# Kernel tuning notes

Measured on AMD Instinct MI355X. Metric: run time of the kernel, lower is better.

## Reference

```python
import jax, jax.numpy as jnp
import numpy as np
import math


def _alibi_slopes(n_heads):
    ratio = 2.0 ** (-8.0 / n_heads)
    return jnp.asarray([ratio ** i for i in range(1, n_heads + 1)], dtype=jnp.float32)


def setup_inputs() -> dict:
    key = jax.random.key(0)
    k1, k2, k3 = jax.random.split(key, 3)
    B, T, D = 2, 2048, 1024
    x = jax.random.normal(k1, (B, T, D), dtype=jnp.float32)
    W_qkv = jax.random.normal(k2, (3 * D, D), dtype=jnp.float32) * (1.0 / math.sqrt(D))
    W_out = jax.random.normal(k3, (D, D), dtype=jnp.float32) * (1.0 / math.sqrt(D))
    return {"x": x, "W_qkv": W_qkv, "W_out": W_out, "n_heads": 16}


def reference(x, W_qkv, W_out, n_heads):
    B, T, D = x.shape
    H = n_heads
    hd = D // H
    scale = 1.0 / math.sqrt(hd)

    # qkv projection: torch Linear computes x @ W.T ; W_qkv is [3D, D]
    qkv = jnp.einsum('btd,ed->bte', x, W_qkv)            # [B, T, 3D]
    qkv = qkv.reshape(B, T, 3, H, hd)
    q = jnp.transpose(qkv[:, :, 0], (0, 2, 1, 3))        # [B, H, T, hd]
    k = jnp.transpose(qkv[:, :, 1], (0, 2, 1, 3))
    v = jnp.transpose(qkv[:, :, 2], (0, 2, 1, 3))

    attn = jnp.einsum('bhqd,bhkd->bhqk', q, k) * scale   # [B, H, T, T]

    pos = jnp.arange(T)
    dist = jnp.abs(pos[None, :] - pos[:, None])          # [T, T]
    slopes = _alibi_slopes(H)                            # [H]
    attn = attn - slopes[None, :, None, None] * dist[None, None, :, :]

    causal = pos[None, :] > pos[:, None]                 # True above diagonal
    attn = jnp.where(causal[None, None, :, :], -jnp.inf, attn)
    attn = jax.nn.softmax(attn, axis=-1)

    out = jnp.einsum('bhqk,bhkd->bhqd', attn, v)         # [B, H, T, hd]
    out = jnp.transpose(out, (0, 2, 1, 3)).reshape(B, T, D)
    return jnp.einsum('btd,ed->bte', out, W_out)         # out projection
```

## Files before the change

### kernel.cpp

```cpp
#include <hip/hip_runtime.h>
#include <hip/hip_bf16.h>
#include <stdint.h>

typedef __attribute__((ext_vector_type(8))) short bf16x8;
typedef __attribute__((ext_vector_type(4))) short short4v;
typedef __attribute__((ext_vector_type(4))) float f32x4;

#define DEV static __device__ __forceinline__

DEV void load_lds16(const void* g, void* l) {
  __builtin_amdgcn_global_load_lds((const __attribute__((address_space(1))) char*)g,
                                   (__attribute__((address_space(3))) char*)l, 16, 0, 0);
}

DEV short f32_to_bf16_bits(float x) {
  union { __hip_bfloat16 h; short s; } u;
  u.h = __float2bfloat16(x);
  return u.s;
}
DEV float bf16_bits_to_f32(short s) {
  union { float f; unsigned u; } u;
  u.u = ((unsigned)(unsigned short)s) << 16;
  return u.f;
}

template<int CTRL>
DEV float dpp_fmax(float x) {
  union { float f; int i; } u, v;
  u.f = x;
  v.i = __builtin_amdgcn_update_dpp(0, u.i, CTRL, 0xf, 0xf, true);
  return fmaxf(x, v.f);
}
DEV float row16_max(float x) {
  x = dpp_fmax<0xB1>(x);
  x = dpp_fmax<0x4E>(x);
  x = dpp_fmax<0x124>(x);
  x = dpp_fmax<0x128>(x);
  return x;
}

#define NX4 1048576
#define NQ4 786432
#define NW4 262144
__global__ __launch_bounds__(256) void conv_f32_bf16(const float4* __restrict__ x,
                                                     const float4* __restrict__ wq,
                                                     const float4* __restrict__ wo,
                                                     short4v* __restrict__ ox,
                                                     short4v* __restrict__ oq,
                                                     short4v* __restrict__ ow) {
  int i = blockIdx.x * 256 + threadIdx.x;
  const float4* src; short4v* dst; int j;
  if (i < NX4)            { src = x;  dst = ox; j = i; }
  else if (i < NX4 + NQ4) { src = wq; dst = oq; j = i - NX4; }
  else                    { src = wo; dst = ow; j = i - NX4 - NQ4; }
  float4 v = src[j];
  short4v s;
  s[0] = f32_to_bf16_bits(v.x); s[1] = f32_to_bf16_bits(v.y);
  s[2] = f32_to_bf16_bits(v.z); s[3] = f32_to_bf16_bits(v.w);
  dst[j] = s;
}

template<bool CF32>
__global__ __launch_bounds__(256) void gemm_bt(const __hip_bfloat16* __restrict__ A,
                                               const __hip_bfloat16* __restrict__ Bt,
                                               void* __restrict__ Cp,
                                               int M, int N, int K) {
  __shared__ short sA[128 * 64];
  __shared__ short sB[128 * 64];
  const int tid = threadIdx.x;
  const int lane = tid & 63;
  const int w = tid >> 6;
  const int wr = w >> 1, wc = w & 1;
  const int l15 = lane & 15, l4 = lane >> 4;
  const long m0 = (long)blockIdx.y * 128, n0 = (long)blockIdx.x * 128;

  f32x4 acc[4][4] = {};

  for (int k0 = 0; k0 < K; k0 += 64) {
    __syncthreads();
#pragma unroll
    for (int c = 0; c < 4; ++c) {
      int ci = c * 256 + tid;
      int row = ci >> 3;
      int sc = (ci & 7) ^ (row & 7);
      load_lds16(A + (m0 + row) * (long)K + k0 + sc * 8, (char*)sA + c * 4096 + w * 1024);
    }
#pragma unroll
    for (int c = 0; c < 4; ++c) {
      int ci = c * 256 + tid;
      int row = ci >> 3;
      int sc = (ci & 7) ^ (row & 7);
      load_lds16(Bt + (n0 + row) * (long)K + k0 + sc * 8, (char*)sB + c * 4096 + w * 1024);
    }
    __syncthreads();
#pragma unroll
    for (int ks = 0; ks < 2; ++ks) {
      bf16x8 av[4], bv[4];
#pragma unroll
      for (int i = 0; i < 4; ++i) {
        int row = wr * 64 + i * 16 + l15;
        int ch = (ks * 4 + l4) ^ (row & 7);
        av[i] = *(const bf16x8*)((const char*)sA + row * 128 + ch * 16);
      }
#pragma unroll
      for (int i = 0; i < 4; ++i) {
        int row = wc * 64 + i * 16 + l15;
        int ch = (ks * 4 + l4) ^ (row & 7);
        bv[i] = *(const bf16x8*)((const char*)sB + row * 128 + ch * 16);
      }
#pragma unroll
      for (int mi = 0; mi < 4; ++mi)
#pragma unroll
        for (int ni = 0; ni < 4; ++ni)
          acc[mi][ni] = __builtin_amdgcn_mfma_f32_16x16x32_bf16(av[mi], bv[ni], acc[mi][ni], 0, 0, 0);
    }
  }
#pragma unroll
  for (int mi = 0; mi < 4; ++mi)
#pragma unroll
    for (int r = 0; r < 4; ++r) {
      long row = m0 + wr * 64 + mi * 16 + l4 * 4 + r;
#pragma unroll
      for (int ni = 0; ni < 4; ++ni) {
        long col = n0 + wc * 64 + ni * 16 + l15;
        if constexpr (CF32)
          ((float*)Cp)[row * (long)N + col] = acc[mi][ni][r];
        else
          ((__hip_bfloat16*)Cp)[row * (long)N + col] = __float2bfloat16(acc[mi][ni][r]);
      }
    }
}

__global__ __launch_bounds__(256) void gemm_bt64(const __hip_bfloat16* __restrict__ A,
                                                 const __hip_bfloat16* __restrict__ Bt,
                                                 float* __restrict__ C,
                                                 int M, int N, int K) {
  __shared__ short sA[64 * 64];
  __shared__ short sB[128 * 64];
  const int tid = threadIdx.x;
  const int lane = tid & 63;
  const int w = tid >> 6;
  const int l15 = lane & 15, l4 = lane >> 4;
  const long m0 = (long)blockIdx.y * 64, n0 = (long)blockIdx.x * 128;

  f32x4 acc[4][2] = {};

  for (int k0 = 0; k0 < K; k0 += 64) {
    __syncthreads();
#pragma unroll
    for (int c = 0; c < 2; ++c) {
      int ci = c * 256 + tid;
      int row = ci >> 3;
      int sc = (ci & 7) ^ (row & 7);
      load_lds16(A + (m0 + row) * (long)K + k0 + sc * 8, (char*)sA + c * 4096 + w * 1024);
    }
#pragma unroll
    for (int c = 0; c < 4; ++c) {
      int ci = c * 256 + tid;
      int row = ci >> 3;
      int sc = (ci & 7) ^ (row & 7);
      load_lds16(Bt + (n0 + row) * (long)K + k0 + sc * 8, (char*)sB + c * 4096 + w * 1024);
    }
    __syncthreads();
#pragma unroll
    for (int ks = 0; ks < 2; ++ks) {
      bf16x8 av[4], bv[2];
#pragma unroll
      for (int i = 0; i < 4; ++i) {
        int row = i * 16 + l15;
        int ch = (ks * 4 + l4) ^ (row & 7);
        av[i] = *(const bf16x8*)((const char*)sA + row * 128 + ch * 16);
      }
#pragma unroll
      for (int i = 0; i < 2; ++i) {
        int row = w * 32 + i * 16 + l15;
        int ch = (ks * 4 + l4) ^ (row & 7);
        bv[i] = *(const bf16x8*)((const char*)sB + row * 128 + ch * 16);
      }
#pragma unroll
      for (int mi = 0; mi < 4; ++mi)
#pragma unroll
        for (int ni = 0; ni < 2; ++ni)
          acc[mi][ni] = __builtin_amdgcn_mfma_f32_16x16x32_bf16(av[mi], bv[ni], acc[mi][ni], 0, 0, 0);
    }
  }
#pragma unroll
  for (int mi = 0; mi < 4; ++mi)
#pragma unroll
    for (int r = 0; r < 4; ++r) {
      long row = m0 + mi * 16 + l4 * 4 + r;
#pragma unroll
      for (int ni = 0; ni < 2; ++ni) {
        long col = n0 + w * 32 + ni * 16 + l15;
        C[row * (long)N + col] = acc[mi][ni][r];
      }
    }
}

__global__ __launch_bounds__(256) void attn_fwd(const __hip_bfloat16* __restrict__ qkv,
                                                __hip_bfloat16* __restrict__ O) {
  constexpr int T = 2048;
  constexpr int LDQ = 3072;
  const int b = blockIdx.x >> 4;
  const int h = blockIdx.x & 15;
  const int q0 = (31 - (int)blockIdx.y) * 64;
  const int tid = threadIdx.x;
  const int lane = tid & 63;
  const int w = tid >> 6;
  const int l15 = lane & 15, l4 = lane >> 4;

  __shared__ short sK[64 * 64];
  __shared__ short sVT[64 * 72];
  __shared__ short sP[4][16 * 72];

  const float sl2 = exp2f(-0.5f * (float)(h + 1)) * 1.44269504f;
  const long base_bt = (long)b * T;

  bf16x8 qf[2];
#pragma unroll
  for (int ks = 0; ks < 2; ++ks) {
    long qrow = base_bt + q0 + w * 16 + l15;
    bf16x8 v = *(const bf16x8*)(qkv + qrow * LDQ + h * 64 + ks * 32 + l4 * 8);
#pragma unroll
    for (int j = 0; j < 8; ++j)
      v[j] = f32_to_bf16_bits(bf16_bits_to_f32(v[j]) * 0.18033688f);
    qf[ks] = v;
  }

  bf16x8 ones;
#pragma unroll
  for (int j = 0; j < 8; ++j) ones[j] = (short)0x3F80;

  f32x4 oacc[4] = {};
  f32x4 lacc = {};
  float mrun[4];
#pragma unroll
  for (int r = 0; r < 4; ++r) mrun[r] = -1e30f;

  for (int kv0 = q0; kv0 >= 0; kv0 -= 64) {
    const bool masked = (kv0 == q0);
    __syncthreads();
#pragma unroll
    for (int c = 0; c < 2; ++c) {
      int ci = c * 256 + tid;
      int row = ci >> 3;
      int sc = (ci & 7) ^ (row & 7);
      load_lds16(qkv + (base_bt + kv0 + row) * LDQ + 1024 + h * 64 + sc * 8,
                 (char*)sK + c * 4096 + w * 1024);
    }
#pragma unroll
    for (int i = 0; i < 2; ++i) {
      int d0 = 8 * (w + 4 * i);
      bf16x8 v = *(const bf16x8*)(qkv + (base_bt + kv0 + lane) * LDQ + 2048 + h * 64 + d0);
#pragma unroll
      for (int j = 0; j < 8; ++j)
        sVT[(d0 + j) * 72 + lane] = v[j];
    }
    __syncthreads();

    f32x4 s[4] = {};
#pragma unroll
    for (int ks = 0; ks < 2; ++ks) {
      bf16x8 kf[4];
#pragma unroll
      for (int nf = 0; nf < 4; ++nf) {
        int row = nf * 16 + l15;
        int ch = (ks * 4 + l4) ^ (row & 7);
        kf[nf] = *(const bf16x8*)((const char*)sK + row * 128 + ch * 16);
      }
#pragma unroll
      for (int nf = 0; nf < 4; ++nf)
        s[nf] = __builtin_amdgcn_mfma_f32_16x16x32_bf16(qf[ks], kf[nf], s[nf], 0, 0, 0);
    }

    float mx[4];
#pragma unroll
    for (int r = 0; r < 4; ++r) {
#pragma unroll
      for (int nf = 0; nf < 4; ++nf) {
        float val = s[nf][r] + sl2 * (float)(kv0 + nf * 16 + l15);
        if (masked) {
          int qloc = w * 16 + l4 * 4 + r;
          val = (nf * 16 + l15 <= qloc) ? val : -1e30f;
        }
        s[nf][r] = val;
      }
      float m4 = fmaxf(fmaxf(s[0][r], s[1][r]), fmaxf(s[2][r], s[3][r]));
      mx[r] = row16_max(m4);
    }

    bool grow = (mx[0] > mrun[0]) | (mx[1] > mrun[1]) |
                (mx[2] > mrun[2]) | (mx[3] > mrun[3]);
    if (__any(grow ? 1 : 0)) {
#pragma unroll
      for (int r = 0; r < 4; ++r) {
        float mnew = fmaxf(mrun[r], mx[r]);
        float f = exp2f(mrun[r] - mnew);
        mrun[r] = mnew;
        lacc[r] *= f;
#pragma unroll
        for (int nd = 0; nd < 4; ++nd)
          oacc[nd][r] *= f;
      }
    }

#pragma unroll
    for (int r = 0; r < 4; ++r) {
      int qloc = l4 * 4 + r;
#pragma unroll
      for (int nf = 0; nf < 4; ++nf) {
        float p = exp2f(s[nf][r] - mrun[r]);
        sP[w][qloc * 72 + nf * 16 + l15] = f32_to_bf16_bits(p);
      }
    }

    asm volatile("s_waitcnt lgkmcnt(0)" ::: "memory");
    __builtin_amdgcn_sched_barrier(0);

#pragma unroll
    for (int ks = 0; ks < 2; ++ks) {
      bf16x8 pf = *(const bf16x8*)(sP[w] + l15 * 72 + ks * 32 + l4 * 8);
      lacc = __builtin_amdgcn_mfma_f32_16x16x32_bf16(pf, ones, lacc, 0, 0, 0);
      bf16x8 vf[4];
#pragma unroll
      for (int nd = 0; nd < 4; ++nd)
        vf[nd] = *(const bf16x8*)(sVT + (nd * 16 + l15) * 72 + ks * 32 + l4 * 8);
#pragma unroll
      for (int nd = 0; nd < 4; ++nd)
        oacc[nd] = __builtin_amdgcn_mfma_f32_16x16x32_bf16(pf, vf[nd], oacc[nd], 0, 0, 0);
    }
  }

#pragma unroll
  for (int r = 0; r < 4; ++r) {
    long q = base_bt + q0 + w * 16 + l4 * 4 + r;
    float inv = 1.0f / lacc[r];
#pragma unroll
    for (int nd = 0; nd < 4; ++nd) {
      int d = nd * 16 + l15;
      O[q * 1024 + h * 64 + d] = __float2bfloat16(oacc[nd][r] * inv);
    }
  }
}

extern "C" void kernel_launch(void* const* d_in, const int* in_sizes, int n_in,
                              void* d_out, int out_size, void* d_ws, size_t ws_size,
                              hipStream_t stream) {
  const float* x    = (const float*)d_in[0];
  const float* Wqkv = (const float*)d_in[1];
  const float* Wout = (const float*)d_in[2];
  float* out = (float*)d_out;

  short* xb  = (short*)d_ws;
  short* wqb = xb + 4194304;
  short* wob = wqb + 3145728;
  short* qkv = wob + 1048576;
  short* attn = xb;

  dim3 blk(256);
  conv_f32_bf16<<<8192, blk, 0, stream>>>((const float4*)x, (const float4*)Wqkv,
                                          (const float4*)Wout, (short4v*)xb,
                                          (short4v*)wqb, (short4v*)wob);
  gemm_bt<false><<<dim3(24, 32), blk, 0, stream>>>((const __hip_bfloat16*)xb,
                                                   (const __hip_bfloat16*)wqb,
                                                   qkv, 4096, 3072, 1024);
  attn_fwd<<<dim3(32, 32), blk, 0, stream>>>((const __hip_bfloat16*)qkv,
                                             (__hip_bfloat16*)attn);
  gemm_bt64<<<dim3(8, 64), blk, 0, stream>>>((const __hip_bfloat16*)attn,
                                             (const __hip_bfloat16*)wob,
                                             out, 4096, 1024, 1024);
}
```

Measured before the change: 188.4 us.

## Double-buffer K/V tiles in attention and prefetch next tile during compute

Switches the attention kernel's K and V^T shared-memory tiles to double buffers. The next tile's K goes in via async global-to-LDS loads and V is held in registers while the current tile is computed, so load latency overlaps with the MFMA and softmax work. It also folds the ALiBi bias into the initial accumulator of the QK MFMA and rescales the running max lazily, only when it grows by more than 8. This costs double the LDS use and some extra registers, and lazy rescaling risks larger intermediate exponent values.

After: 186.6 us. Within noise of the previous version (-0.9%).

```diff
diff --git a/kernel.cpp b/kernel.cpp
--- a/kernel.cpp
+++ b/kernel.cpp
@@ -209,12 +209,29 @@
   const int w = tid >> 6;
   const int l15 = lane & 15, l4 = lane >> 4;
 
-  __shared__ short sK[64 * 64];
-  __shared__ short sVT[64 * 72];
+  __shared__ short sK[2][64 * 64];
+  __shared__ short sVT[2][64 * 72];
   __shared__ short sP[4][16 * 72];
 
   const float sl2 = exp2f(-0.5f * (float)(h + 1)) * 1.44269504f;
   const long base_bt = (long)b * T;
+
+  const __hip_bfloat16* Kbase = qkv + base_bt * LDQ + 1024 + h * 64;
+  const __hip_bfloat16* Vbase = qkv + base_bt * LDQ + 2048 + h * 64;
+
+  long koff[2];  size_t kdst_off[2];
+#pragma unroll
+  for (int c = 0; c < 2; ++c) {
+    int ci = c * 256 + tid;
+    int row = ci >> 3;
+    int sc = (ci & 7) ^ (row & 7);
+    koff[c] = (long)row * LDQ + sc * 8;
+    kdst_off[c] = (size_t)(c * 4096 + w * 1024);
+  }
+  long voff[2];
+#pragma unroll
+  for (int i = 0; i < 2; ++i)
+    voff[i] = (long)lane * LDQ + 8 * (w + 4 * i);
 
   bf16x8 qf[2];
 #pragma unroll
@@ -237,28 +254,49 @@
 #pragma unroll
   for (int r = 0; r < 4; ++r) mrun[r] = -1e30f;
 
+  bf16x8 vreg[2];
+  {
+    const __hip_bfloat16* Kt = Kbase + (long)q0 * LDQ;
+    const __hip_bfloat16* Vt = Vbase + (long)q0 * LDQ;
+#pragma unroll
+    for (int c = 0; c < 2; ++c)
+      load_lds16(Kt + koff[c], (char*)sK[0] + kdst_off[c]);
+#pragma unroll
+    for (int i = 0; i < 2; ++i)
+      vreg[i] = *(const bf16x8*)(Vt + voff[i]);
+    asm volatile("s_waitcnt vmcnt(0)" ::: "memory");
+#pragma unroll
+    for (int i = 0; i < 2; ++i) {
+      int d0 = 8 * (w + 4 * i);
+#pragma unroll
+      for (int j = 0; j < 8; ++j)
+        sVT[0][(d0 + j) * 72 + lane] = vreg[i][j];
+    }
+  }
+
+  int cur = 0;
   for (int kv0 = q0; kv0 >= 0; kv0 -= 64) {
     const bool masked = (kv0 == q0);
+    const bool have_next = (kv0 > 0);
     __syncthreads();
-#pragma unroll
-    for (int c = 0; c < 2; ++c) {
-      int ci = c * 256 + tid;
-      int row = ci >> 3;
-      int sc = (ci & 7) ^ (row & 7);
-      load_lds16(qkv + (base_bt + kv0 + row) * LDQ + 1024 + h * 64 + sc * 8,
-                 (char*)sK + c * 4096 + w * 1024);
-    }
-#pragma unroll
-    for (int i = 0; i < 2; ++i) {
-      int d0 = 8 * (w + 4 * i);
-      bf16x8 v = *(const bf16x8*)(qkv + (base_bt + kv0 + lane) * LDQ + 2048 + h * 64 + d0);
-#pragma unroll
-      for (int j = 0; j < 8; ++j)
-        sVT[(d0 + j) * 72 + lane] = v[j];
-    }
-    __syncthreads();
-
-    f32x4 s[4] = {};
+
+    if (have_next) {
+      const __hip_bfloat16* Kt = Kbase + (long)(kv0 - 64) * LDQ;
+      const __hip_bfloat16* Vt = Vbase + (long)(kv0 - 64) * LDQ;
+#pragma unroll
+      for (int c = 0; c < 2; ++c)
+        load_lds16(Kt + koff[c], (char*)sK[cur ^ 1] + kdst_off[c]);
+#pragma unroll
+      for (int i = 0; i < 2; ++i)
+        vreg[i] = *(const bf16x8*)(Vt + voff[i]);
+    }
+
+    f32x4 s[4];
+#pragma unroll
+    for (int nf = 0; nf < 4; ++nf) {
+      float al = sl2 * (float)(kv0 + nf * 16 + l15);
+      s[nf] = f32x4{al, al, al, al};
+    }
 #pragma unroll
     for (int ks = 0; ks < 2; ++ks) {
       bf16x8 kf[4];
@@ -266,7 +304,7 @@
       for (int nf = 0; nf < 4; ++nf) {
         int row = nf * 16 + l15;
         int ch = (ks * 4 + l4) ^ (row & 7);
-        kf[nf] = *(const bf16x8*)((const char*)sK + row * 128 + ch * 16);
+        kf[nf] = *(const bf16x8*)((const char*)sK[cur] + row * 128 + ch * 16);
       }
 #pragma unroll
       for (int nf = 0; nf < 4; ++nf)
@@ -276,21 +314,18 @@
     float mx[4];
 #pragma unroll
     for (int r = 0; r < 4; ++r) {
-#pragma unroll
-      for (int nf = 0; nf < 4; ++nf) {
-        float val = s[nf][r] + sl2 * (float)(kv0 + nf * 16 + l15);
-        if (masked) {
-          int qloc = w * 16 + l4 * 4 + r;
-          val = (nf * 16 + l15 <= qloc) ? val : -1e30f;
-        }
-        s[nf][r] = val;
+      if (masked) {
+        int qloc = w * 16 + l4 * 4 + r;
+#pragma unroll
+        for (int nf = 0; nf < 4; ++nf)
+          s[nf][r] = (nf * 16 + l15 <= qloc) ? s[nf][r] : -1e30f;
       }
       float m4 = fmaxf(fmaxf(s[0][r], s[1][r]), fmaxf(s[2][r], s[3][r]));
       mx[r] = row16_max(m4);
     }
 
-    bool grow = (mx[0] > mrun[0]) | (mx[1] > mrun[1]) |
-                (mx[2] > mrun[2]) | (mx[3] > mrun[3]);
+    bool grow = (mx[0] > mrun[0] + 8.f) | (mx[1] > mrun[1] + 8.f) |
+                (mx[2] > mrun[2] + 8.f) | (mx[3] > mrun[3] + 8.f);
     if (__any(grow ? 1 : 0)) {
 #pragma unroll
       for (int r = 0; r < 4; ++r) {
@@ -324,11 +359,23 @@
       bf16x8 vf[4];
 #pragma unroll
       for (int nd = 0; nd < 4; ++nd)
-        vf[nd] = *(const bf16x8*)(sVT + (nd * 16 + l15) * 72 + ks * 32 + l4 * 8);
+        vf[nd] = *(const bf16x8*)(sVT[cur] + (nd * 16 + l15) * 72 + ks * 32 + l4 * 8);
 #pragma unroll
       for (int nd = 0; nd < 4; ++nd)
         oacc[nd] = __builtin_amdgcn_mfma_f32_16x16x32_bf16(pf, vf[nd], oacc[nd], 0, 0, 0);
     }
+
+    if (have_next) {
+      asm volatile("s_waitcnt vmcnt(0)" ::: "memory");
+#pragma unroll
+      for (int i = 0; i < 2; ++i) {
+        int d0 = 8 * (w + 4 * i);
+#pragma unroll
+        for (int j = 0; j < 8; ++j)
+          sVT[cur ^ 1][(d0 + j) * 72 + lane] = vreg[i][j];
+      }
+    }
+    cur ^= 1;
   }
 
 #pragma unroll
```

## Transpose score MFMA, fold ALiBi bias into accumulator init, lazy max rescale

Applied to the files above, without the earlier changes.

Swaps the MFMA operand order so each lane holds one query row across key columns. Row max then needs only two cross-lane shuffles instead of a DPP reduction, and P is written to LDS as packed 8-byte stores. The ALiBi bias is precomputed per lane and loaded as the MFMA accumulator initial value, which removes per-element adds. The running max is rescaled only when the new max exceeds the old one by more than 8 (log2 domain). This cuts rescale work but lets unnormalized exponentials grow up to 2^8 before renormalization, which could affect bf16 precision.

Measured after the change: 185.1 us. About the same (-1.8%).

```diff
diff --git a/kernel.cpp b/kernel.cpp
--- a/kernel.cpp
+++ b/kernel.cpp
@@ -5,6 +5,7 @@
 typedef __attribute__((ext_vector_type(8))) short bf16x8;
 typedef __attribute__((ext_vector_type(4))) short short4v;
 typedef __attribute__((ext_vector_type(4))) float f32x4;
+typedef __attribute__((ext_vector_type(2))) unsigned int uint2v;
 
 #define DEV static __device__ __forceinline__
 
@@ -22,21 +23,6 @@
   union { float f; unsigned u; } u;
   u.u = ((unsigned)(unsigned short)s) << 16;
   return u.f;
-}
-
-template<int CTRL>
-DEV float dpp_fmax(float x) {
-  union { float f; int i; } u, v;
-  u.f = x;
-  v.i = __builtin_amdgcn_update_dpp(0, u.i, CTRL, 0xf, 0xf, true);
-  return fmaxf(x, v.f);
-}
-DEV float row16_max(float x) {
-  x = dpp_fmax<0xB1>(x);
-  x = dpp_fmax<0x4E>(x);
-  x = dpp_fmax<0x124>(x);
-  x = dpp_fmax<0x128>(x);
-  return x;
 }
 
 #define NX4 1048576
@@ -227,15 +213,20 @@
     qf[ks] = v;
   }
 
+  f32x4 alinv[4];
+#pragma unroll
+  for (int nf = 0; nf < 4; ++nf)
+#pragma unroll
+    for (int r = 0; r < 4; ++r)
+      alinv[nf][r] = sl2 * (float)(nf * 16 + l4 * 4 + r);
+
   bf16x8 ones;
 #pragma unroll
   for (int j = 0; j < 8; ++j) ones[j] = (short)0x3F80;
 
   f32x4 oacc[4] = {};
   f32x4 lacc = {};
-  float mrun[4];
-#pragma unroll
-  for (int r = 0; r < 4; ++r) mrun[r] = -1e30f;
+  float mrun = -1e30f;
 
   for (int kv0 = q0; kv0 >= 0; kv0 -= 64) {
     const bool masked = (kv0 == q0);
@@ -258,7 +249,14 @@
     }
     __syncthreads();
 
-    f32x4 s[4] = {};
+    float skv0 = sl2 * (float)kv0;
+    f32x4 s[4];
+#pragma unroll
+    for (int nf = 0; nf < 4; ++nf) {
+#pragma unroll
+      for (int r = 0; r < 4; ++r)
+        s[nf][r] = alinv[nf][r] + skv0;
+    }
 #pragma unroll
     for (int ks = 0; ks < 2; ++ks) {
       bf16x8 kf[4];
@@ -270,48 +268,53 @@
       }
 #pragma unroll
       for (int nf = 0; nf < 4; ++nf)
-        s[nf] = __builtin_amdgcn_mfma_f32_16x16x32_bf16(qf[ks], kf[nf], s[nf], 0, 0, 0);
-    }
-
-    float mx[4];
-#pragma unroll
-    for (int r = 0; r < 4; ++r) {
-#pragma unroll
-      for (int nf = 0; nf < 4; ++nf) {
-        float val = s[nf][r] + sl2 * (float)(kv0 + nf * 16 + l15);
-        if (masked) {
-          int qloc = w * 16 + l4 * 4 + r;
-          val = (nf * 16 + l15 <= qloc) ? val : -1e30f;
-        }
-        s[nf][r] = val;
-      }
-      float m4 = fmaxf(fmaxf(s[0][r], s[1][r]), fmaxf(s[2][r], s[3][r]));
-      mx[r] = row16_max(m4);
-    }
-
-    bool grow = (mx[0] > mrun[0]) | (mx[1] > mrun[1]) |
-                (mx[2] > mrun[2]) | (mx[3] > mrun[3]);
-    if (__any(grow ? 1 : 0)) {
+        s[nf] = __builtin_amdgcn_mfma_f32_16x16x32_bf16(kf[nf], qf[ks], s[nf], 0, 0, 0);
+    }
+
+    if (masked) {
+      int qloc = w * 16 + l15;
+#pragma unroll
+      for (int nf = 0; nf < 4; ++nf)
+#pragma unroll
+        for (int r = 0; r < 4; ++r)
+          s[nf][r] = (nf * 16 + l4 * 4 + r <= qloc) ? s[nf][r] : -1e30f;
+    }
+
+    float mx = fmaxf(fmaxf(fmaxf(s[0][0], s[0][1]), fmaxf(s[0][2], s[0][3])),
+                     fmaxf(fmaxf(s[1][0], s[1][1]), fmaxf(s[1][2], s[1][3])));
+    float mx2 = fmaxf(fmaxf(fmaxf(s[2][0], s[2][1]), fmaxf(s[2][2], s[2][3])),
+                      fmaxf(fmaxf(s[3][0], s[3][1]), fmaxf(s[3][2], s[3][3])));
+    mx = fmaxf(mx, mx2);
+    mx = fmaxf(mx, __shfl_xor(mx, 16, 64));
+    mx = fmaxf(mx, __shfl_xor(mx, 32, 64));
+
+    if (__any((mx > mrun + 8.f) ? 1 : 0)) {
+      float mnew = fmaxf(mrun, mx);
+      float f = exp2f(mrun - mnew);
+      mrun = mnew;
+      float ff[4];
+#pragma unroll
+      for (int r = 0; r < 4; ++r)
+        ff[r] = __shfl(f, l4 * 4 + r, 64);
 #pragma unroll
       for (int r = 0; r < 4; ++r) {
-        float mnew = fmaxf(mrun[r], mx[r]);
-        float f = exp2f(mrun[r] - mnew);
-        mrun[r] = mnew;
-        lacc[r] *= f;
+        lacc[r] *= ff[r];
 #pragma unroll
         for (int nd = 0; nd < 4; ++nd)
-          oacc[nd][r] *= f;
-      }
-    }
-
-#pragma unroll
-    for (int r = 0; r < 4; ++r) {
-      int qloc = l4 * 4 + r;
-#pragma unroll
-      for (int nf = 0; nf < 4; ++nf) {
-        float p = exp2f(s[nf][r] - mrun[r]);
-        sP[w][qloc * 72 + nf * 16 + l15] = f32_to_bf16_bits(p);
-      }
+          oacc[nd][r] *= ff[r];
+      }
+    }
+
+#pragma unroll
+    for (int nf = 0; nf < 4; ++nf) {
+      unsigned p0 = (unsigned)(unsigned short)f32_to_bf16_bits(exp2f(s[nf][0] - mrun));
+      unsigned p1 = (unsigned)(unsigned short)f32_to_bf16_bits(exp2f(s[nf][1] - mrun));
+      unsigned p2 = (unsigned)(unsigned short)f32_to_bf16_bits(exp2f(s[nf][2] - mrun));
+      unsigned p3 = (unsigned)(unsigned short)f32_to_bf16_bits(exp2f(s[nf][3] - mrun));
+      uint2v u;
+      u[0] = p0 | (p1 << 16);
+      u[1] = p2 | (p3 << 16);
+      *(uint2v*)(sP[w] + l15 * 72 + nf * 16 + l4 * 4) = u;
     }
 
     asm volatile("s_waitcnt lgkmcnt(0)" ::: "memory");
```
